# Kernel optimization log

Measured on AMD Instinct MI355X. Metric: run time of the kernel, lower is better.

The kernel has to match this reference:

```python
import jax, jax.numpy as jnp
import numpy as np

VAR_CXCY = 0.1   # SSD encoding variances
VAR_WH = 0.2
THRESH = 0.5     # match threshold from forward()
EPS = 1e-6


def point_form(p):
    """[P,4] (cx,cy,w,h) -> (x1,y1,x2,y2)."""
    return jnp.concatenate([p[..., :2] - p[..., 2:] / 2,
                            p[..., :2] + p[..., 2:] / 2], axis=-1)


def iou(a, b):
    """a: [N,4] xyxy, b: [P,4] xyxy -> [N,P] jaccard overlap."""
    lt = jnp.maximum(a[:, None, :2], b[None, :, :2])
    rb = jnp.minimum(a[:, None, 2:], b[None, :, 2:])
    wh = jnp.clip(rb - lt, 0.0)
    inter = wh[..., 0] * wh[..., 1]
    area_a = (a[:, 2] - a[:, 0]) * (a[:, 3] - a[:, 1])
    area_b = (b[:, 2] - b[:, 0]) * (b[:, 3] - b[:, 1])
    return inter / (area_a[:, None] + area_b[None, :] - inter + EPS)


def match_one(gt, labels, priors, priors_pt):
    """SSD match for a single image.
    gt: [N,4] xyxy, labels: [N] int, priors: [P,4] cxcywh, priors_pt: [P,4] xyxy.
    Returns loc targets [P,4] and conf targets [P] (0 = background).
    """
    ov = iou(gt, priors_pt)                       # [N,P]
    best_prior_idx = jnp.argmax(ov, axis=1)        # [N] best prior per gt
    best_truth_ov = jnp.max(ov, axis=0)            # [P]
    best_truth_idx = jnp.argmax(ov, axis=0)        # [P] best gt per prior
    n = gt.shape[0]
    # ensure every gt keeps its best prior
    best_truth_ov = best_truth_ov.at[best_prior_idx].set(2.0)
    best_truth_idx = best_truth_idx.at[best_prior_idx].set(jnp.arange(n))
    matches = gt[best_truth_idx]                   # [P,4]
    conf = labels[best_truth_idx] + 1              # shift so 0 = background
    conf = jnp.where(best_truth_ov < THRESH, 0, conf)
    # encode matched boxes relative to priors
    m_cxcy = (matches[:, :2] + matches[:, 2:]) * 0.5
    m_wh = jnp.clip(matches[:, 2:] - matches[:, :2], EPS)
    g_cxcy = (m_cxcy - priors[:, :2]) / (VAR_CXCY * priors[:, 2:])
    g_wh = jnp.log(m_wh / priors[:, 2:]) / VAR_WH
    return jnp.concatenate([g_cxcy, g_wh], axis=1), conf


def setup_inputs() -> dict:
    key = jax.random.key(0)
    k1, k2, k3, k4, k5 = jax.random.split(key, 5)
    B, N, P = 32, 100, 8732
    # ground-truth boxes: valid xyxy corners in [0,1]
    xy1 = jax.random.uniform(k1, (B, N, 2)) * 0.7
    wh = 0.05 + jax.random.uniform(k2, (B, N, 2)) * 0.25
    gt_boxes = jnp.concatenate([xy1, xy1 + wh], axis=-1).astype(jnp.float32)
    gt_labels = jax.random.randint(k3, (B, N), 0, 20)
    # priors: cxcywh
    p_cxcy = jax.random.uniform(k4, (P, 2))
    p_wh = 0.05 + jax.random.uniform(k5, (P, 2)) * 0.45
    priors = jnp.concatenate([p_cxcy, p_wh], axis=-1).astype(jnp.float32)
    return {"gt_boxes": gt_boxes, "gt_labels": gt_labels, "priors": priors}


def reference(gt_boxes, gt_labels, priors):
    priors_pt = point_form(priors)
    loc_t, conf_t = jax.vmap(
        lambda g, l: match_one(g, l, priors, priors_pt))(gt_boxes, gt_labels)
    return loc_t, conf_t
```

## Files before the change

kernel.cpp:

```cpp
#include <hip/hip_runtime.h>

#pragma clang fp contract(off)

#define BB 32
#define NN 100
#define PP 8732
#define CH 16
#define LDW 257
#define NBX 35

template <bool USE_PART>
__global__ __launch_bounds__(256) void k_iou_pass(
    const float* __restrict__ gt,
    const float* __restrict__ priors,
    unsigned long long* __restrict__ red,
    unsigned char* __restrict__ m8)
{
    __shared__ unsigned int s_iou[CH * LDW];
    __shared__ unsigned long long s_part[NN][17];
    __shared__ float s_area[NN];

    const int b = blockIdx.y;
    const int t = threadIdx.x;
    const int p = blockIdx.x * 256 + t;
    const bool valid = p < PP;
    const int pc = valid ? p : (PP - 1);

    const float4* __restrict__ gtb =
        reinterpret_cast<const float4*>(gt) + b * NN;

    if (t < NN) {
        float4 g = gtb[t];
        s_area[t] = (g.z - g.x) * (g.w - g.y);
    }

    const float4 pr = reinterpret_cast<const float4*>(priors)[pc];
    const float px1 = pr.x - pr.z * 0.5f;
    const float py1 = pr.y - pr.w * 0.5f;
    const float px2 = pr.x + pr.z * 0.5f;
    const float py2 = pr.y + pr.w * 0.5f;
    const float area_b = (px2 - px1) * (py2 - py1);

    float best_ov = -1.0f;
    int best_j = 0;

    __syncthreads();

    for (int jc = 0; jc < NN; jc += CH) {
        const int nr = (NN - jc) < CH ? (NN - jc) : CH;

        #pragma unroll
        for (int jj = 0; jj < CH; ++jj) {
            if (jj >= nr) break;
            float4 g = gtb[jc + jj];
            float area_a = s_area[jc + jj];
            float ltx = fmaxf(g.x, px1), lty = fmaxf(g.y, py1);
            float rbx = fminf(g.z, px2), rby = fminf(g.w, py2);
            float w = fmaxf(rbx - ltx, 0.0f), h = fmaxf(rby - lty, 0.0f);
            float inter = w * h;
            float iou = inter / (area_a + area_b - inter + 1e-6f);
            if (iou > best_ov) { best_ov = iou; best_j = jc + jj; }
            s_iou[jj * LDW + t] = __float_as_uint(iou);
        }
        __syncthreads();

        {
            const int r = t & 15;
            const int s = t >> 4;
            if (r < nr) {
                const unsigned int* row = s_iou + r * LDW + s * 16;
                unsigned int bb = row[0];
                int bi = 0;
                #pragma unroll
                for (int i = 1; i < 16; ++i) {
                    unsigned int v = row[i];
                    if (v > bb) { bb = v; bi = i; }
                }
                int pw = blockIdx.x * 256 + s * 16 + bi;
                s_part[jc + r][s] = ((unsigned long long)bb << 32) |
                                    (unsigned int)(~pw);
            }
        }
        __syncthreads();
    }

    if (t < NN) {
        unsigned long long best = s_part[t][0];
        #pragma unroll
        for (int s = 1; s < 16; ++s) {
            unsigned long long k = s_part[t][s];
            if (k > best) best = k;
        }
        if (USE_PART) {
            red[((size_t)b * NBX + blockIdx.x) * NN + t] = best;
        } else {
            atomicMax(&red[b * NN + t], best);
        }
    }
    if (valid) {
        m8[b * PP + p] =
            (unsigned char)(best_j | ((best_ov < 0.5f) ? 0x80 : 0));
    }
}

template <bool USE_PART>
__global__ __launch_bounds__(256) void k_encode(
    const float* __restrict__ gt,
    const int*   __restrict__ labels,
    const float* __restrict__ priors,
    const unsigned long long* __restrict__ red,
    const unsigned char* __restrict__ m8,
    float* __restrict__ loc_out,
    float* __restrict__ conf_out)
{
    __shared__ int s_forced[256];

    const int b = blockIdx.y;
    const int t = threadIdx.x;
    const int p = blockIdx.x * 256 + t;

    s_forced[t] = -1;
    __syncthreads();
    if (t < NN) {
        unsigned long long best;
        if (USE_PART) {
            const unsigned long long* q = red + (size_t)b * NBX * NN + t;
            best = q[0];
            #pragma unroll 5
            for (int bx = 1; bx < NBX; ++bx) {
                unsigned long long k = q[(size_t)bx * NN];
                if (k > best) best = k;
            }
        } else {
            best = red[b * NN + t];
        }
        int kp = (int)~(unsigned int)(best & 0xFFFFFFFFull);
        int lp = kp - blockIdx.x * 256;
        if ((unsigned)lp < 256u) atomicMax(&s_forced[lp], t);
    }
    __syncthreads();

    if (p >= PP) return;
    const int forced_j = s_forced[t];

    const unsigned char m = m8[b * PP + p];
    const int j    = (forced_j >= 0) ? forced_j : (m & 0x7f);
    const int lab  = labels[b * NN + j];
    const int conf = (forced_j < 0 && (m & 0x80)) ? 0 : (lab + 1);

    const float4 pr = reinterpret_cast<const float4*>(priors)[p];
    const float4 g  = reinterpret_cast<const float4*>(gt)[b * NN + j];
    const float mcx = (g.x + g.z) * 0.5f;
    const float mcy = (g.y + g.w) * 0.5f;
    const float mw  = fmaxf(g.z - g.x, 1e-6f);
    const float mh  = fmaxf(g.w - g.y, 1e-6f);
    const float gcx = (mcx - pr.x) / (0.1f * pr.z);
    const float gcy = (mcy - pr.y) / (0.1f * pr.w);
    const float gw  = logf(mw / pr.z) / 0.2f;
    const float gh  = logf(mh / pr.w) / 0.2f;

    reinterpret_cast<float4*>(loc_out)[b * PP + p] =
        make_float4(gcx, gcy, gw, gh);
    conf_out[b * PP + p] = (float)conf;
}

extern "C" void kernel_launch(void* const* d_in, const int* in_sizes, int n_in,
                              void* d_out, int out_size, void* d_ws, size_t ws_size,
                              hipStream_t stream) {
    const float* gt     = (const float*)d_in[0];
    const int*   labels = (const int*)  d_in[1];
    const float* priors = (const float*)d_in[2];

    float* loc  = (float*)d_out;
    float* conf = (float*)d_out + (size_t)BB * PP * 4;

    const size_t part_bytes = (size_t)BB * NBX * NN * 8;
    const size_t m8_bytes   = (size_t)BB * PP;
    dim3 grid(NBX, BB);

    if (ws_size >= part_bytes + m8_bytes) {
        unsigned long long* part = (unsigned long long*)d_ws;
        unsigned char* m8 = (unsigned char*)d_ws + part_bytes;
        k_iou_pass<true><<<grid, 256, 0, stream>>>(gt, priors, part, m8);
        k_encode<true><<<grid, 256, 0, stream>>>(gt, labels, priors, part,
                                                 m8, loc, conf);
    } else {
        unsigned long long* gkey = (unsigned long long*)d_ws;
        unsigned char* m8 = (unsigned char*)d_ws + (size_t)BB * NN * 8;
        hipMemsetAsync(gkey, 0, (size_t)BB * NN * 8, stream);
        k_iou_pass<false><<<grid, 256, 0, stream>>>(gt, priors, gkey, m8);
        k_encode<false><<<grid, 256, 0, stream>>>(gt, labels, priors, gkey,
                                                  m8, loc, conf);
    }
}
```

Baseline: 96.40 us.

## Replace shared-memory chunked argmax with wavefront shuffle reduction per gt

Removes the chunked shared-memory staging of IoU values and the two block-wide barriers per chunk. Each gt's best prior is now found with a 64-lane butterfly shuffle max plus a ballot to pick the lowest winning lane, and lane 0 writes one partial per wavefront. This cuts the shared-memory footprint and the per-block partial count from 16 to 4. In exchange it runs six shuffles and a ballot for every gt on every thread, which may cost more ALU and cross-lane work than the old strided scan. Clamped out-of-range lanes in the last block now take part in the max, but they hold duplicates of the last valid prior, so the winner and tie-break stay correct.

```diff
diff --git a/kernel.cpp b/kernel.cpp
--- a/kernel.cpp
+++ b/kernel.cpp
@@ -5,8 +5,6 @@
 #define BB 32
 #define NN 100
 #define PP 8732
-#define CH 16
-#define LDW 257
 #define NBX 35
 
 template <bool USE_PART>
@@ -16,9 +14,8 @@
     unsigned long long* __restrict__ red,
     unsigned char* __restrict__ m8)
 {
-    __shared__ unsigned int s_iou[CH * LDW];
-    __shared__ unsigned long long s_part[NN][17];
     __shared__ float s_area[NN];
+    __shared__ unsigned long long s_part[NN][5];
 
     const int b = blockIdx.y;
     const int t = threadIdx.x;
@@ -44,51 +41,46 @@
     float best_ov = -1.0f;
     int best_j = 0;
 
+    const int wbase = blockIdx.x * 256 + (t & ~63);
+    const int wid = t >> 6;
+    const bool lane0 = (t & 63) == 0;
+
     __syncthreads();
 
-    for (int jc = 0; jc < NN; jc += CH) {
-        const int nr = (NN - jc) < CH ? (NN - jc) : CH;
+    #pragma unroll 4
+    for (int j = 0; j < NN; ++j) {
+        float4 g = gtb[j];
+        float area_a = s_area[j];
+        float ltx = fmaxf(g.x, px1), lty = fmaxf(g.y, py1);
+        float rbx = fminf(g.z, px2), rby = fminf(g.w, py2);
+        float w = fmaxf(rbx - ltx, 0.0f), h = fmaxf(rby - lty, 0.0f);
+        float inter = w * h;
+        float iou = inter / (area_a + area_b - inter + 1e-6f);
 
-        #pragma unroll
-        for (int jj = 0; jj < CH; ++jj) {
-            if (jj >= nr) break;
-            float4 g = gtb[jc + jj];
-            float area_a = s_area[jc + jj];
-            float ltx = fmaxf(g.x, px1), lty = fmaxf(g.y, py1);
-            float rbx = fminf(g.z, px2), rby = fminf(g.w, py2);
-            float w = fmaxf(rbx - ltx, 0.0f), h = fmaxf(rby - lty, 0.0f);
-            float inter = w * h;
-            float iou = inter / (area_a + area_b - inter + 1e-6f);
-            if (iou > best_ov) { best_ov = iou; best_j = jc + jj; }
-            s_iou[jj * LDW + t] = __float_as_uint(iou);
+        if (iou > best_ov) { best_ov = iou; best_j = j; }
+
+        float m = iou;
+        m = fmaxf(m, __shfl_xor(m, 1));
+        m = fmaxf(m, __shfl_xor(m, 2));
+        m = fmaxf(m, __shfl_xor(m, 4));
+        m = fmaxf(m, __shfl_xor(m, 8));
+        m = fmaxf(m, __shfl_xor(m, 16));
+        m = fmaxf(m, __shfl_xor(m, 32));
+        unsigned long long win = __ballot(iou == m);
+        int lmin = __ffsll((long long)win) - 1;
+        if (lane0) {
+            s_part[j][wid] =
+                ((unsigned long long)__float_as_uint(m) << 32) |
+                (unsigned int)(~(wbase + lmin));
         }
-        __syncthreads();
-
-        {
-            const int r = t & 15;
-            const int s = t >> 4;
-            if (r < nr) {
-                const unsigned int* row = s_iou + r * LDW + s * 16;
-                unsigned int bb = row[0];
-                int bi = 0;
-                #pragma unroll
-                for (int i = 1; i < 16; ++i) {
-                    unsigned int v = row[i];
-                    if (v > bb) { bb = v; bi = i; }
-                }
-                int pw = blockIdx.x * 256 + s * 16 + bi;
-                s_part[jc + r][s] = ((unsigned long long)bb << 32) |
-                                    (unsigned int)(~pw);
-            }
-        }
-        __syncthreads();
     }
+    __syncthreads();
 
     if (t < NN) {
         unsigned long long best = s_part[t][0];
         #pragma unroll
-        for (int s = 1; s < 16; ++s) {
-            unsigned long long k = s_part[t][s];
+        for (int w = 1; w < 4; ++w) {
+            unsigned long long k = s_part[t][w];
             if (k > best) best = k;
         }
         if (USE_PART) {
```

Result: slower. 114.8 us (+19.1%).

## Split IoU pass over two GT halves per block with 128 priors each

Applied to the files above, without the earlier changes.

The IoU pass now gives each 256-thread block 128 priors, and the two thread halves each handle 50 of the 100 ground-truth boxes. Per-prior best matches from the two halves are merged through shared memory. This doubles the number of IoU blocks (69 per image instead of 35) to raise parallelism and cut the serial per-thread GT loop. In exchange there are more partial-reduction rows for the encode kernel to scan (69 instead of 35) and an extra merge step with a barrier.

```diff
diff --git a/kernel.cpp b/kernel.cpp
--- a/kernel.cpp
+++ b/kernel.cpp
@@ -5,9 +5,13 @@
 #define BB 32
 #define NN 100
 #define PP 8732
+#define BPB 128
+#define HALF 50
 #define CH 16
-#define LDW 257
-#define NBX 35
+#define LDW2 129
+#define NSEG 8
+#define NBX 69
+#define EBX 35
 
 template <bool USE_PART>
 __global__ __launch_bounds__(256) void k_iou_pass(
@@ -16,15 +20,19 @@
     unsigned long long* __restrict__ red,
     unsigned char* __restrict__ m8)
 {
-    __shared__ unsigned int s_iou[CH * LDW];
-    __shared__ unsigned long long s_part[NN][17];
+    __shared__ unsigned int s_iou[2 * CH][LDW2];
+    __shared__ unsigned long long s_part[NN][NSEG + 1];
     __shared__ float s_area[NN];
+    __shared__ unsigned long long s_cmerge[BPB];
 
     const int b = blockIdx.y;
     const int t = threadIdx.x;
-    const int p = blockIdx.x * 256 + t;
+    const int h  = t >> 7;
+    const int pl = t & 127;
+    const int p = blockIdx.x * BPB + pl;
     const bool valid = p < PP;
     const int pc = valid ? p : (PP - 1);
+    const int j0 = h * HALF;
 
     const float4* __restrict__ gtb =
         reinterpret_cast<const float4*>(gt) + b * NN;
@@ -46,29 +54,32 @@
 
     __syncthreads();
 
-    for (int jc = 0; jc < NN; jc += CH) {
-        const int nr = (NN - jc) < CH ? (NN - jc) : CH;
+    for (int jc = 0; jc < HALF; jc += CH) {
+        const int nr = (HALF - jc) < CH ? (HALF - jc) : CH;
 
         #pragma unroll
         for (int jj = 0; jj < CH; ++jj) {
             if (jj >= nr) break;
-            float4 g = gtb[jc + jj];
-            float area_a = s_area[jc + jj];
+            const int j = j0 + jc + jj;
+            float4 g = gtb[j];
+            float area_a = s_area[j];
             float ltx = fmaxf(g.x, px1), lty = fmaxf(g.y, py1);
             float rbx = fminf(g.z, px2), rby = fminf(g.w, py2);
-            float w = fmaxf(rbx - ltx, 0.0f), h = fmaxf(rby - lty, 0.0f);
-            float inter = w * h;
+            float w = fmaxf(rbx - ltx, 0.0f), h2 = fmaxf(rby - lty, 0.0f);
+            float inter = w * h2;
             float iou = inter / (area_a + area_b - inter + 1e-6f);
-            if (iou > best_ov) { best_ov = iou; best_j = jc + jj; }
-            s_iou[jj * LDW + t] = __float_as_uint(iou);
+            if (iou > best_ov) { best_ov = iou; best_j = j; }
+            s_iou[h * CH + jj][pl] = __float_as_uint(iou);
         }
         __syncthreads();
 
         {
-            const int r = t & 15;
-            const int s = t >> 4;
-            if (r < nr) {
-                const unsigned int* row = s_iou + r * LDW + s * 16;
+            const int r = t & 31;
+            const int s = t >> 5;
+            const int rr = r & 15;
+            const int rh = r >> 4;
+            if (rr < nr) {
+                const unsigned int* row = &s_iou[r][s * 16];
                 unsigned int bb = row[0];
                 int bi = 0;
                 #pragma unroll
@@ -76,18 +87,35 @@
                     unsigned int v = row[i];
                     if (v > bb) { bb = v; bi = i; }
                 }
-                int pw = blockIdx.x * 256 + s * 16 + bi;
-                s_part[jc + r][s] = ((unsigned long long)bb << 32) |
-                                    (unsigned int)(~pw);
+                int pw = blockIdx.x * BPB + s * 16 + bi;
+                s_part[rh * HALF + jc + rr][s] =
+                    ((unsigned long long)bb << 32) | (unsigned int)(~pw);
             }
         }
         __syncthreads();
+    }
+
+    if (h == 1) {
+        s_cmerge[pl] = ((unsigned long long)__float_as_uint(best_ov) << 32) |
+                       (unsigned int)best_j;
+    }
+    __syncthreads();
+
+    if (h == 0) {
+        unsigned long long k1 = s_cmerge[pl];
+        float ov1 = __uint_as_float((unsigned int)(k1 >> 32));
+        int   j1  = (int)(k1 & 0xFFFFFFFFull);
+        if (ov1 > best_ov) { best_ov = ov1; best_j = j1; }
+        if (valid) {
+            m8[b * PP + p] =
+                (unsigned char)(best_j | ((best_ov < 0.5f) ? 0x80 : 0));
+        }
     }
 
     if (t < NN) {
         unsigned long long best = s_part[t][0];
         #pragma unroll
-        for (int s = 1; s < 16; ++s) {
+        for (int s = 1; s < NSEG; ++s) {
             unsigned long long k = s_part[t][s];
             if (k > best) best = k;
         }
@@ -96,10 +124,6 @@
         } else {
             atomicMax(&red[b * NN + t], best);
         }
-    }
-    if (valid) {
-        m8[b * PP + p] =
-            (unsigned char)(best_j | ((best_ov < 0.5f) ? 0x80 : 0));
     }
 }
 
@@ -126,7 +150,7 @@
         if (USE_PART) {
             const unsigned long long* q = red + (size_t)b * NBX * NN + t;
             best = q[0];
-            #pragma unroll 5
+            #pragma unroll 4
             for (int bx = 1; bx < NBX; ++bx) {
                 unsigned long long k = q[(size_t)bx * NN];
                 if (k > best) best = k;
@@ -176,20 +200,21 @@
 
     const size_t part_bytes = (size_t)BB * NBX * NN * 8;
     const size_t m8_bytes   = (size_t)BB * PP;
-    dim3 grid(NBX, BB);
+    dim3 grid_i(NBX, BB);
+    dim3 grid_e(EBX, BB);
 
     if (ws_size >= part_bytes + m8_bytes) {
         unsigned long long* part = (unsigned long long*)d_ws;
         unsigned char* m8 = (unsigned char*)d_ws + part_bytes;
-        k_iou_pass<true><<<grid, 256, 0, stream>>>(gt, priors, part, m8);
-        k_encode<true><<<grid, 256, 0, stream>>>(gt, labels, priors, part,
-                                                 m8, loc, conf);
+        k_iou_pass<true><<<grid_i, 256, 0, stream>>>(gt, priors, part, m8);
+        k_encode<true><<<grid_e, 256, 0, stream>>>(gt, labels, priors, part,
+                                                   m8, loc, conf);
     } else {
         unsigned long long* gkey = (unsigned long long*)d_ws;
         unsigned char* m8 = (unsigned char*)d_ws + (size_t)BB * NN * 8;
         hipMemsetAsync(gkey, 0, (size_t)BB * NN * 8, stream);
-        k_iou_pass<false><<<grid, 256, 0, stream>>>(gt, priors, gkey, m8);
-        k_encode<false><<<grid, 256, 0, stream>>>(gt, labels, priors, gkey,
-                                                  m8, loc, conf);
+        k_iou_pass<false><<<grid_i, 256, 0, stream>>>(gt, priors, gkey, m8);
+        k_encode<false><<<grid_e, 256, 0, stream>>>(gt, labels, priors, gkey,
+                                                    m8, loc, conf);
     }
 }
```

New measurement: 95.57 us (median of 2 runs). About the same (-0.9%).

## Fuse box encoding into IoU pass and patch forced matches in small kernel

Applied to the files above, without the earlier changes.

The encode step moves into the IoU kernel, so each prior writes its loc and conf targets right after finding its best ground truth. This removes the intermediate per-prior match byte array and a full second pass over all priors. A tiny follow-up kernel with one block per image reduces the per-gt best-prior keys and overwrites only the forced-match priors, with the highest gt index winning duplicates to mimic scatter semantics. The cost is a per-prior gather of labels and gt inside the heavier kernel, plus an O(N^2) duplicate check in shared memory.

```diff
diff --git a/kernel.cpp b/kernel.cpp
--- a/kernel.cpp
+++ b/kernel.cpp
@@ -10,11 +10,13 @@
 #define NBX 35
 
 template <bool USE_PART>
-__global__ __launch_bounds__(256) void k_iou_pass(
+__global__ __launch_bounds__(256) void k_match_enc(
     const float* __restrict__ gt,
     const float* __restrict__ priors,
+    const int*   __restrict__ labels,
     unsigned long long* __restrict__ red,
-    unsigned char* __restrict__ m8)
+    float* __restrict__ loc_out,
+    float* __restrict__ conf_out)
 {
     __shared__ unsigned int s_iou[CH * LDW];
     __shared__ unsigned long long s_part[NN][17];
@@ -97,30 +99,41 @@
             atomicMax(&red[b * NN + t], best);
         }
     }
+
     if (valid) {
-        m8[b * PP + p] =
-            (unsigned char)(best_j | ((best_ov < 0.5f) ? 0x80 : 0));
+        const int lab  = labels[b * NN + best_j];
+        const int conf = (best_ov < 0.5f) ? 0 : (lab + 1);
+
+        const float4 g = gtb[best_j];
+        const float mcx = (g.x + g.z) * 0.5f;
+        const float mcy = (g.y + g.w) * 0.5f;
+        const float mw  = fmaxf(g.z - g.x, 1e-6f);
+        const float mh  = fmaxf(g.w - g.y, 1e-6f);
+        const float gcx = (mcx - pr.x) / (0.1f * pr.z);
+        const float gcy = (mcy - pr.y) / (0.1f * pr.w);
+        const float gw  = logf(mw / pr.z) / 0.2f;
+        const float gh  = logf(mh / pr.w) / 0.2f;
+
+        reinterpret_cast<float4*>(loc_out)[b * PP + p] =
+            make_float4(gcx, gcy, gw, gh);
+        conf_out[b * PP + p] = (float)conf;
     }
 }
 
 template <bool USE_PART>
-__global__ __launch_bounds__(256) void k_encode(
+__global__ __launch_bounds__(128) void k_patch(
     const float* __restrict__ gt,
+    const float* __restrict__ priors,
     const int*   __restrict__ labels,
-    const float* __restrict__ priors,
     const unsigned long long* __restrict__ red,
-    const unsigned char* __restrict__ m8,
     float* __restrict__ loc_out,
     float* __restrict__ conf_out)
 {
-    __shared__ int s_forced[256];
-
-    const int b = blockIdx.y;
+    __shared__ int s_pstar[NN];
+
+    const int b = blockIdx.x;
     const int t = threadIdx.x;
-    const int p = blockIdx.x * 256 + t;
-
-    s_forced[t] = -1;
-    __syncthreads();
+
     if (t < NN) {
         unsigned long long best;
         if (USE_PART) {
@@ -134,34 +147,33 @@
         } else {
             best = red[b * NN + t];
         }
-        int kp = (int)~(unsigned int)(best & 0xFFFFFFFFull);
-        int lp = kp - blockIdx.x * 256;
-        if ((unsigned)lp < 256u) atomicMax(&s_forced[lp], t);
+        s_pstar[t] = (int)~(unsigned int)(best & 0xFFFFFFFFull);
     }
     __syncthreads();
 
-    if (p >= PP) return;
-    const int forced_j = s_forced[t];
-
-    const unsigned char m = m8[b * PP + p];
-    const int j    = (forced_j >= 0) ? forced_j : (m & 0x7f);
-    const int lab  = labels[b * NN + j];
-    const int conf = (forced_j < 0 && (m & 0x80)) ? 0 : (lab + 1);
-
-    const float4 pr = reinterpret_cast<const float4*>(priors)[p];
-    const float4 g  = reinterpret_cast<const float4*>(gt)[b * NN + j];
-    const float mcx = (g.x + g.z) * 0.5f;
-    const float mcy = (g.y + g.w) * 0.5f;
-    const float mw  = fmaxf(g.z - g.x, 1e-6f);
-    const float mh  = fmaxf(g.w - g.y, 1e-6f);
-    const float gcx = (mcx - pr.x) / (0.1f * pr.z);
-    const float gcy = (mcy - pr.y) / (0.1f * pr.w);
-    const float gw  = logf(mw / pr.z) / 0.2f;
-    const float gh  = logf(mh / pr.w) / 0.2f;
-
-    reinterpret_cast<float4*>(loc_out)[b * PP + p] =
-        make_float4(gcx, gcy, gw, gh);
-    conf_out[b * PP + p] = (float)conf;
+    if (t < NN) {
+        const int p = s_pstar[t];
+        bool win = true;
+        for (int j2 = t + 1; j2 < NN; ++j2)
+            if (s_pstar[j2] == p) { win = false; break; }
+        if (win) {
+            const float4 g =
+                reinterpret_cast<const float4*>(gt)[b * NN + t];
+            const float4 pr = reinterpret_cast<const float4*>(priors)[p];
+            const float mcx = (g.x + g.z) * 0.5f;
+            const float mcy = (g.y + g.w) * 0.5f;
+            const float mw  = fmaxf(g.z - g.x, 1e-6f);
+            const float mh  = fmaxf(g.w - g.y, 1e-6f);
+            const float gcx = (mcx - pr.x) / (0.1f * pr.z);
+            const float gcy = (mcy - pr.y) / (0.1f * pr.w);
+            const float gw  = logf(mw / pr.z) / 0.2f;
+            const float gh  = logf(mh / pr.w) / 0.2f;
+
+            reinterpret_cast<float4*>(loc_out)[b * PP + p] =
+                make_float4(gcx, gcy, gw, gh);
+            conf_out[b * PP + p] = (float)(labels[b * NN + t] + 1);
+        }
+    }
 }
 
 extern "C" void kernel_launch(void* const* d_in, const int* in_sizes, int n_in,
@@ -175,21 +187,20 @@
     float* conf = (float*)d_out + (size_t)BB * PP * 4;
 
     const size_t part_bytes = (size_t)BB * NBX * NN * 8;
-    const size_t m8_bytes   = (size_t)BB * PP;
     dim3 grid(NBX, BB);
 
-    if (ws_size >= part_bytes + m8_bytes) {
+    if (ws_size >= part_bytes) {
         unsigned long long* part = (unsigned long long*)d_ws;
-        unsigned char* m8 = (unsigned char*)d_ws + part_bytes;
-        k_iou_pass<true><<<grid, 256, 0, stream>>>(gt, priors, part, m8);
-        k_encode<true><<<grid, 256, 0, stream>>>(gt, labels, priors, part,
-                                                 m8, loc, conf);
+        k_match_enc<true><<<grid, 256, 0, stream>>>(gt, priors, labels,
+                                                    part, loc, conf);
+        k_patch<true><<<BB, 128, 0, stream>>>(gt, priors, labels,
+                                              part, loc, conf);
     } else {
         unsigned long long* gkey = (unsigned long long*)d_ws;
-        unsigned char* m8 = (unsigned char*)d_ws + (size_t)BB * NN * 8;
         hipMemsetAsync(gkey, 0, (size_t)BB * NN * 8, stream);
-        k_iou_pass<false><<<grid, 256, 0, stream>>>(gt, priors, gkey, m8);
-        k_encode<false><<<grid, 256, 0, stream>>>(gt, labels, priors, gkey,
-                                                  m8, loc, conf);
+        k_match_enc<false><<<grid, 256, 0, stream>>>(gt, priors, labels,
+                                                     gkey, loc, conf);
+        k_patch<false><<<BB, 128, 0, stream>>>(gt, priors, labels,
+                                               gkey, loc, conf);
     }
 }
```

New measurement: 103.0 us. 1.07x slower.
